# Performance work log

Measured on AMD Instinct MI355X. Metric: run time of the kernel, lower is better.

The kernel has to match this reference:

```python
import jax, jax.numpy as jnp
import numpy as np

N = 50000
E = 800000
IN = 128
HID = 128
OUT = 128
HEADS = 8
EPS = 1e-5
NEG_SLOPE = 0.2


def _gat_conv(x, src, dst, W, a_src, a_dst, b, concat):
    """PyG-style GATConv (eval mode, self-loops already appended to src/dst).
    W: [Fin, H*C], a_src/a_dst: [H, C], b: [H*C] or [C]."""
    n = x.shape[0]
    H, C = a_src.shape
    h = (x @ W).reshape(n, H, C)                      # [N,H,C]
    al_s = jnp.einsum('nhc,hc->nh', h, a_src)         # [N,H]
    al_d = jnp.einsum('nhc,hc->nh', h, a_dst)         # [N,H]
    e = jax.nn.leaky_relu(al_s[src] + al_d[dst], NEG_SLOPE)  # [E',H]
    m = jax.ops.segment_max(e, dst, num_segments=n)   # per-dst softmax (stable)
    ex = jnp.exp(e - m[dst])
    s = jax.ops.segment_sum(ex, dst, num_segments=n)
    alpha = ex / s[dst]                               # [E',H]
    out = jax.ops.segment_sum(h[src] * alpha[..., None], dst, num_segments=n)
    out = out.reshape(n, H * C) if concat else out[:, 0, :]
    return out + b


def _layernorm(x, g, b):
    mu = x.mean(-1, keepdims=True)
    var = ((x - mu) ** 2).mean(-1, keepdims=True)
    return (x - mu) * jax.lax.rsqrt(var + EPS) * g + b


def setup_inputs() -> dict:
    key = jax.random.key(0)
    ks = jax.random.split(key, 24)
    d = {}
    d['x'] = jax.random.normal(ks[0], (N, IN), jnp.float32)
    d['edge_index'] = jax.random.randint(ks[1], (2, E), 0, N)
    C = HID // HEADS
    # layer 0: in -> hidden, 8 heads, concat
    d['W0'] = jax.random.normal(ks[2], (IN, HID)) * 0.05
    d['a_src0'] = jax.random.normal(ks[3], (HEADS, C)) * 0.05
    d['a_dst0'] = jax.random.normal(ks[4], (HEADS, C)) * 0.05
    d['b0'] = jnp.zeros((HID,), jnp.float32)
    d['g0'] = jnp.ones((HID,), jnp.float32)
    d['be0'] = jnp.zeros((HID,), jnp.float32)
    # layer 1: hidden -> hidden, 8 heads, concat
    d['W1'] = jax.random.normal(ks[5], (HID, HID)) * 0.05
    d['a_src1'] = jax.random.normal(ks[6], (HEADS, C)) * 0.05
    d['a_dst1'] = jax.random.normal(ks[7], (HEADS, C)) * 0.05
    d['b1'] = jnp.zeros((HID,), jnp.float32)
    d['g1'] = jnp.ones((HID,), jnp.float32)
    d['be1'] = jnp.zeros((HID,), jnp.float32)
    # layer 2: hidden -> out, 1 head, no concat
    d['W2'] = jax.random.normal(ks[8], (HID, OUT)) * 0.05
    d['a_src2'] = jax.random.normal(ks[9], (1, OUT)) * 0.05
    d['a_dst2'] = jax.random.normal(ks[10], (1, OUT)) * 0.05
    d['b2'] = jnp.zeros((OUT,), jnp.float32)
    d['g2'] = jnp.ones((OUT,), jnp.float32)
    d['be2'] = jnp.zeros((OUT,), jnp.float32)
    return d


def reference(x, edge_index, W0, a_src0, a_dst0, b0, g0, be0,
              W1, a_src1, a_dst1, b1, g1, be1,
              W2, a_src2, a_dst2, b2, g2, be2):
    n = x.shape[0]
    loops = jnp.arange(n)
    src = jnp.concatenate([edge_index[0], loops])  # add self-loops (PyG default)
    dst = jnp.concatenate([edge_index[1], loops])

    h = _gat_conv(x, src, dst, W0, a_src0, a_dst0, b0, concat=True)
    h = jax.nn.elu(_layernorm(h, g0, be0))          # dropout: eval mode -> identity
    h = _gat_conv(h, src, dst, W1, a_src1, a_dst1, b1, concat=True)
    h = jax.nn.elu(_layernorm(h, g1, be1))
    h = _gat_conv(h, src, dst, W2, a_src2, a_dst2, b2, concat=False)
    h = _layernorm(h, g2, be2)
    return h
```

## Files before the change

kernel.cpp:

```cpp
#include <hip/hip_runtime.h>
#include <hip/hip_bf16.h>

#define NN 50000
#define EE 800000
#define EP 850000
#define DD 128
#define NB 196

#define NBUCK 196
#define BCAP 8192
#define E_PER_BLK 4096

typedef __attribute__((ext_vector_type(8))) short short8;
typedef __attribute__((ext_vector_type(4))) float f32x4;

__device__ __forceinline__ float bfu(unsigned short u){ return __uint_as_float(((unsigned)u)<<16); }
__device__ __forceinline__ unsigned short f2bs(float x){
  __hip_bfloat16 h = __float2bfloat16(x);
  union { __hip_bfloat16 h; unsigned short u; } cv; cv.h = h; return cv.u;
}

__global__ void __launch_bounds__(256) prep_kernel(
    const float* __restrict__ W0, const float* __restrict__ as0, const float* __restrict__ ad0,
    const float* __restrict__ W1, const float* __restrict__ as1, const float* __restrict__ ad1,
    const float* __restrict__ W2, const float* __restrict__ as2, const float* __restrict__ ad2,
    unsigned short* __restrict__ Wmf, int* __restrict__ bcur)
{
  const int tid = threadIdx.x;
  if (blockIdx.x == 0 && tid < NBUCK) bcur[tid] = 0;
  if (blockIdx.x < 24){
    const int L = blockIdx.x >> 3, seg = blockIdx.x & 7;
    const float* W = (L == 0) ? W0 : (L == 1) ? W1 : W2;
    int idx = seg*256 + tid;
    int t = idx >> 6, lane = idx & 63;
    int c = t >> 2, kb = t & 3;
    int m = lane & 15, quad = lane >> 4;
    unsigned short out[8];
    #pragma unroll
    for (int j = 0; j < 8; j++){
      int k = kb*32 + quad*8 + j;
      out[j] = f2bs(W[(size_t)k*DD + c*16 + m]);
    }
    *(uint4*)&Wmf[(((size_t)L*36 + t)*64 + lane)*8] = *(const uint4*)out;
  } else if (blockIdx.x < 120){
    const int q = blockIdx.x - 24;
    const int wIdx = q*4 + (tid >> 6);
    const int L = wIdx >> 7, k = wIdx & 127;
    const float *W, *as, *ad; int H;
    if (L == 0){ W = W0; as = as0; ad = ad0; H = 8; }
    else if (L == 1){ W = W1; as = as1; ad = ad1; H = 8; }
    else { W = W2; as = as2; ad = ad2; H = 1; }
    const int lane = tid & 63;
    const int c0 = lane*2;
    float w0 = W[(size_t)k*DD + c0];
    float w1 = W[(size_t)k*DD + c0 + 1];
    float ps = w0*as[c0] + w1*as[c0+1];
    float pd = w0*ad[c0] + w1*ad[c0+1];
    if (H == 8){
      #pragma unroll
      for (int off = 1; off <= 4; off <<= 1){
        ps += __shfl_xor(ps, off, 64);
        pd += __shfl_xor(pd, off, 64);
      }
    } else {
      #pragma unroll
      for (int off = 1; off <= 32; off <<= 1){
        ps += __shfl_xor(ps, off, 64);
        pd += __shfl_xor(pd, off, 64);
      }
    }
    int srcLane = (lane < 8) ? lane*8 : (lane < 16 ? (lane-8)*8 : 0);
    float vs = __shfl(ps, srcLane, 64);
    float vd = __shfl(pd, srcLane, 64);
    float myv;
    if (H == 8) myv = (lane < 8) ? vs : (lane < 16 ? vd : 0.f);
    else        myv = (lane == 0) ? ps : (lane == 1 ? pd : 0.f);
    const int kb = k >> 5, quad = (k >> 3) & 3, j = k & 7;
    if (lane < 16)
      Wmf[(((size_t)L*36 + 32 + kb)*64 + quad*16 + lane)*8 + j] = f2bs(myv);
  }
}

__global__ void __launch_bounds__(256) binpass1_kernel(const int* __restrict__ ei,
    unsigned int* __restrict__ bins, int* __restrict__ bcur)
{
  __shared__ int h[NBUCK];
  __shared__ int lofs[NBUCK];
  __shared__ int gbase[NBUCK];
  __shared__ unsigned int st[E_PER_BLK];
  __shared__ int buf[256];
  const int tid = threadIdx.x;
  for (int i = tid; i < NBUCK; i += 256) h[i] = 0;
  __syncthreads();

  const int e0 = blockIdx.x * E_PER_BLK;
  unsigned int pk[16];
  #pragma unroll
  for (int k = 0; k < 16; k++){
    int e = e0 + k*256 + tid;
    if (e < EP){
      int s, d;
      if (e < EE){ s = ei[e]; d = ei[EE + e]; } else { s = d = e - EE; }
      int b = d >> 8;
      pk[k] = ((unsigned)s << 16) | ((unsigned)b << 8) | (unsigned)(d & 255);
      atomicAdd(&h[b], 1);
    } else pk[k] = 0xFFFFFFFFu;
  }
  __syncthreads();

  int v = (tid < NBUCK) ? h[tid] : 0;
  buf[tid] = v;
  __syncthreads();
  for (int off = 1; off < 256; off <<= 1){
    int t = (tid >= off) ? buf[tid - off] : 0;
    __syncthreads();
    buf[tid] += t;
    __syncthreads();
  }
  if (tid < NBUCK){
    lofs[tid]  = buf[tid] - v;
    gbase[tid] = (v > 0) ? atomicAdd(&bcur[tid], v) : 0;
    h[tid] = lofs[tid];
  }
  __syncthreads();

  #pragma unroll
  for (int k = 0; k < 16; k++){
    if (pk[k] != 0xFFFFFFFFu){
      int b = (pk[k] >> 8) & 255;
      int p = atomicAdd(&h[b], 1);
      st[p] = pk[k];
    }
  }
  __syncthreads();

  const int total = buf[255];
  for (int i = tid; i < total; i += 256){
    unsigned int p = st[i];
    int b = (p >> 8) & 255;
    int idx = gbase[b] + (i - lofs[b]);
    if (idx < BCAP) bins[(size_t)b * BCAP + idx] = p;
  }
}

__global__ void __launch_bounds__(256) binpass2_kernel(const unsigned int* __restrict__ bins,
    const int* __restrict__ bcur, int* __restrict__ rowStart, unsigned short* __restrict__ srcL)
{
  __shared__ int buf[256];
  __shared__ int lcnt[256];
  __shared__ int lcur[256];
  __shared__ int ebase_s, cnt_s;
  const int b = blockIdx.x;
  const int tid = threadIdx.x;

  int v = (tid < NBUCK) ? bcur[tid] : 0;
  buf[tid] = v;
  lcnt[tid] = 0;
  __syncthreads();
  for (int off = 1; off < 256; off <<= 1){
    int t = (tid >= off) ? buf[tid - off] : 0;
    __syncthreads();
    buf[tid] += t;
    __syncthreads();
  }
  if (tid == b){ ebase_s = buf[tid] - v; cnt_s = v; }
  __syncthreads();
  const int ebase = ebase_s, cnt = cnt_s;
  const unsigned int* mybins = bins + (size_t)b * BCAP;

  for (int i = tid; i < cnt; i += 256)
    atomicAdd(&lcnt[mybins[i] & 255], 1);
  __syncthreads();

  int c = lcnt[tid];
  buf[tid] = c;
  __syncthreads();
  for (int off = 1; off < 256; off <<= 1){
    int t = (tid >= off) ? buf[tid - off] : 0;
    __syncthreads();
    buf[tid] += t;
    __syncthreads();
  }
  int excl = buf[tid] - c;
  int d = (b << 8) + tid;
  if (d <= NN) rowStart[d] = ebase + excl;
  lcur[tid] = ebase + excl;
  __syncthreads();

  for (int i = tid; i < cnt; i += 256){
    unsigned int p = mybins[i];
    int pos = atomicAdd(&lcur[p & 255], 1);
    srcL[pos] = (unsigned short)(p >> 16);
  }
}

template<bool XBF16, int H>
__global__ void __launch_bounds__(256) gemm_mfma_kernel(const void* __restrict__ Xv,
    const unsigned short* __restrict__ Wmf,
    unsigned short* __restrict__ Hout,
    float* __restrict__ alS, float* __restrict__ alD)
{
  __shared__ unsigned short wl[36*64*8];
  const int tid = threadIdx.x;
  {
    const uint4* src = (const uint4*)Wmf;
    uint4* dst = (uint4*)wl;
    #pragma unroll
    for (int i = 0; i < 9; i++)
      dst[tid + i*256] = src[tid + i*256];
  }
  const int lane = tid & 63, wv = tid >> 6;
  const int r0 = blockIdx.x*64 + wv*16;
  const int m = lane & 15, quad = lane >> 4;
  const int row = r0 + m;
  const bool rowOK = row < NN;

  short8 a[4];
  if (XBF16){
    const short* Xb = (const short*)Xv;
    #pragma unroll
    for (int kb = 0; kb < 4; kb++){
      if (rowOK) a[kb] = *(const short8*)&Xb[(size_t)row*DD + kb*32 + quad*8];
      else       a[kb] = (short8){0,0,0,0,0,0,0,0};
    }
  } else {
    const float* Xf = (const float*)Xv;
    #pragma unroll
    for (int kb = 0; kb < 4; kb++){
      if (rowOK){
        float4 f0 = *(const float4*)&Xf[(size_t)row*DD + kb*32 + quad*8];
        float4 f1 = *(const float4*)&Xf[(size_t)row*DD + kb*32 + quad*8 + 4];
        union { short8 v; unsigned short u[8]; } cv;
        cv.u[0]=f2bs(f0.x); cv.u[1]=f2bs(f0.y); cv.u[2]=f2bs(f0.z); cv.u[3]=f2bs(f0.w);
        cv.u[4]=f2bs(f1.x); cv.u[5]=f2bs(f1.y); cv.u[6]=f2bs(f1.z); cv.u[7]=f2bs(f1.w);
        a[kb] = cv.v;
      } else a[kb] = (short8){0,0,0,0,0,0,0,0};
    }
  }
  __syncthreads();

  f32x4 acc[9];
  #pragma unroll
  for (int c = 0; c < 9; c++) acc[c] = (f32x4){0.f,0.f,0.f,0.f};
  #pragma unroll
  for (int c = 0; c < 9; c++){
    #pragma unroll
    for (int kb = 0; kb < 4; kb++){
      short8 b = *(const short8*)&wl[((c*4 + kb)*64 + lane)*8];
      acc[c] = __builtin_amdgcn_mfma_f32_16x16x32_bf16(a[kb], b, acc[c], 0, 0, 0);
    }
  }

  #pragma unroll
  for (int c = 0; c < 8; c++){
    #pragma unroll
    for (int r = 0; r < 4; r++){
      int rw = r0 + quad*4 + r;
      if (rw < NN) Hout[(size_t)rw*DD + c*16 + m] = f2bs(acc[c][r]);
    }
  }
  #pragma unroll
  for (int r = 0; r < 4; r++){
    int rw = r0 + quad*4 + r;
    if (rw < NN){
      float v = acc[8][r];
      if (H == 8){
        if (m < 8) alS[rw*8 + m]       = v;
        else       alD[rw*8 + (m - 8)] = v;
      } else {
        if (m == 0)      alS[rw] = v;
        else if (m == 1) alD[rw] = v;
      }
    }
  }
}

template<int H, bool FINAL>
__global__ void __launch_bounds__(256) aggln_kernel(
    const int* __restrict__ rowStart, const unsigned short* __restrict__ srcL,
    const float* __restrict__ alS, const float* __restrict__ alD,
    const unsigned short* __restrict__ hB,
    const float* __restrict__ b, const float* __restrict__ g, const float* __restrict__ be,
    void* __restrict__ outv)
{
  const int lane = threadIdx.x & 63;
  const int d    = blockIdx.x*4 + (threadIdx.x >> 6);
  const int C    = DD / H;
  const int c0   = lane*2;
  const int hd   = c0 / C;
  const int start = __builtin_amdgcn_readfirstlane(rowStart[d]);
  const int end   = __builtin_amdgcn_readfirstlane(rowStart[d+1]);
  const float aldv = alD[d*H + hd];

  float ssum = 0.f, a0 = 0.f, a1 = 0.f;
  const unsigned int* __restrict__ sw = (const unsigned int*)srcL;

  #define PROC(sv) { \
    int s_ = (sv); \
    const unsigned short* hr_ = hB + (size_t)s_*DD; \
    const float* ar_ = alS + s_*H; \
    unsigned int hw_ = *(const unsigned int*)&hr_[c0]; \
    float e_ = ar_[hd] + aldv; \
    e_ = fmaxf(e_, 0.2f*e_); \
    float w_ = __expf(e_); \
    ssum += w_; \
    a0 = fmaf(__uint_as_float(hw_ << 16),          w_, a0); \
    a1 = fmaf(__uint_as_float(hw_ & 0xFFFF0000u),  w_, a1); \
  }

  int jw = start >> 1;
  if (start & 1){
    unsigned int w = sw[jw]; PROC((int)(w >> 16)); jw++;
  }
  const int jwF = end >> 1;
  for (; jw + 2 <= jwF; jw += 2){
    unsigned int w0 = sw[jw], w1 = sw[jw+1];
    PROC((int)(w0 & 0xFFFFu)); PROC((int)(w0 >> 16));
    PROC((int)(w1 & 0xFFFFu)); PROC((int)(w1 >> 16));
  }
  for (; jw < jwF; ++jw){
    unsigned int w = sw[jw];
    PROC((int)(w & 0xFFFFu)); PROC((int)(w >> 16));
  }
  if (end & 1){
    unsigned int w = sw[jwF]; PROC((int)(w & 0xFFFFu));
  }
  #undef PROC

  const float sinv = 1.f / ssum;

  float v0 = a0*sinv + b[c0], v1 = a1*sinv + b[c0+1];
  float s2 = v0 + v1;
  #pragma unroll
  for (int off = 32; off >= 1; off >>= 1) s2 += __shfl_xor(s2, off, 64);
  float mu = s2 * (1.0f/128.0f);
  float d0 = v0 - mu, d1 = v1 - mu;
  float q = d0*d0 + d1*d1;
  #pragma unroll
  for (int off = 32; off >= 1; off >>= 1) q += __shfl_xor(q, off, 64);
  float r = rsqrtf(q*(1.0f/128.0f) + 1e-5f);
  float y0 = d0*r*g[c0]   + be[c0];
  float y1 = d1*r*g[c0+1] + be[c0+1];
  if (FINAL){
    *(float2*)&((float*)outv)[(size_t)d*DD + c0] = make_float2(y0, y1);
  } else {
    y0 = y0 > 0.f ? y0 : __expf(y0) - 1.f;
    y1 = y1 > 0.f ? y1 : __expf(y1) - 1.f;
    ushort2 o; o.x = f2bs(y0); o.y = f2bs(y1);
    *(ushort2*)&((unsigned short*)outv)[(size_t)d*DD + c0] = o;
  }
}

template<bool XBF16, int H, bool FINAL>
static void run_layer(const void* x, const unsigned short* WmfL,
                      const float* b, const float* g, const float* be,
                      const int* rowStart, const unsigned short* srcL,
                      unsigned short* hB, float* alS, float* alD,
                      void* outv, hipStream_t stream)
{
  gemm_mfma_kernel<XBF16, H><<<782, 256, 0, stream>>>(x, WmfL, hB, alS, alD);
  aggln_kernel<H, FINAL><<<12500, 256, 0, stream>>>(rowStart, srcL, alS, alD, hB,
                                                    b, g, be, outv);
}

extern "C" void kernel_launch(void* const* d_in, const int* in_sizes, int n_in,
                              void* d_out, int out_size, void* d_ws, size_t ws_size,
                              hipStream_t stream)
{
  char* w = (char*)d_ws;
  unsigned short* accB = (unsigned short*)w;     w += (size_t)NN*DD*2;
  unsigned short* hB   = (unsigned short*)w;     w += (size_t)NN*DD*2;
  float* alS      = (float*)w;                   w += (size_t)NN*8*4;
  float* alD      = (float*)w;                   w += (size_t)NN*8*4;
  unsigned short* Wmf = (unsigned short*)w;      w += (size_t)3*36*64*8*2;
  int*   rowStart = (int*)w;                     w += (size_t)(NN+1)*4;
  int*   bcur     = (int*)w;                     w += 1024;
  unsigned short* srcL = (unsigned short*)w;     w += (size_t)EP*2;
  if (ws_size < (size_t)(w - (char*)d_ws)) return;

  unsigned int* bins = (unsigned int*)accB;

  const float* x  = (const float*)d_in[0];
  const int*   ei = (const int*)d_in[1];
  const float *W0=(const float*)d_in[2], *as0=(const float*)d_in[3], *ad0=(const float*)d_in[4];
  const float *b0=(const float*)d_in[5], *g0=(const float*)d_in[6], *be0=(const float*)d_in[7];
  const float *W1=(const float*)d_in[8], *as1=(const float*)d_in[9], *ad1=(const float*)d_in[10];
  const float *b1=(const float*)d_in[11],*g1=(const float*)d_in[12],*be1=(const float*)d_in[13];
  const float *W2=(const float*)d_in[14],*as2=(const float*)d_in[15],*ad2=(const float*)d_in[16];
  const float *b2=(const float*)d_in[17],*g2=(const float*)d_in[18],*be2=(const float*)d_in[19];

  prep_kernel<<<NB, 256, 0, stream>>>(W0, as0, ad0, W1, as1, ad1, W2, as2, ad2, Wmf, bcur);
  binpass1_kernel<<<(EP + E_PER_BLK - 1)/E_PER_BLK, 256, 0, stream>>>(ei, bins, bcur);
  binpass2_kernel<<<NBUCK, 256, 0, stream>>>(bins, bcur, rowStart, srcL);

  run_layer<false, 8, false>(x,    Wmf,            b0, g0, be0,
                             rowStart, srcL, hB, alS, alD, accB, stream);
  run_layer<true, 8, false>(accB, Wmf + (size_t)36*64*8,   b1, g1, be1,
                             rowStart, srcL, hB, alS, alD, accB, stream);
  run_layer<true, 1, true>(accB, Wmf + (size_t)2*36*64*8,  b2, g2, be2,
                             rowStart, srcL, hB, alS, alD, d_out, stream);
}
```

Baseline: 284.0 us.

## Fuse layer-0 GEMM with edge binning pass and batch gather loads in aggregation

The first layer's MFMA GEMM and the first edge-binning pass now run as one launch, with blocks split by index and a shared LDS buffer, so the two independent stages overlap and one launch is saved. The aggregation kernel now loads up to 127 source indices per wave with one coalesced read and broadcasts them with readlane. It then issues eight independent gathers of features and attention scores before doing the math, to raise memory-level parallelism. This costs more registers and relies on the hand-computed LDS offsets and the 127-edge chunk bound being correct.

```diff
diff --git a/kernel.cpp b/kernel.cpp
--- a/kernel.cpp
+++ b/kernel.cpp
@@ -10,6 +10,8 @@
 #define NBUCK 196
 #define BCAP 8192
 #define E_PER_BLK 4096
+#define GEMM_BLKS 782
+#define BP1_BLKS ((EP + E_PER_BLK - 1)/E_PER_BLK)
 
 typedef __attribute__((ext_vector_type(8))) short short8;
 typedef __attribute__((ext_vector_type(4))) float f32x4;
@@ -81,19 +83,19 @@
   }
 }
 
-__global__ void __launch_bounds__(256) binpass1_kernel(const int* __restrict__ ei,
-    unsigned int* __restrict__ bins, int* __restrict__ bcur)
-{
-  __shared__ int h[NBUCK];
-  __shared__ int lofs[NBUCK];
-  __shared__ int gbase[NBUCK];
-  __shared__ unsigned int st[E_PER_BLK];
-  __shared__ int buf[256];
+__device__ __forceinline__ void bp1_body(int bid, const int* __restrict__ ei,
+    unsigned int* __restrict__ bins, int* __restrict__ bcur, char* smem)
+{
+  unsigned int* st = (unsigned int*)smem;
+  int* h     = (int*)(smem + 16384);
+  int* lofs  = (int*)(smem + 17168);
+  int* gbase = (int*)(smem + 17952);
+  int* buf   = (int*)(smem + 18736);
   const int tid = threadIdx.x;
   for (int i = tid; i < NBUCK; i += 256) h[i] = 0;
   __syncthreads();
 
-  const int e0 = blockIdx.x * E_PER_BLK;
+  const int e0 = bid * E_PER_BLK;
   unsigned int pk[16];
   #pragma unroll
   for (int k = 0; k < 16; k++){
@@ -195,12 +197,12 @@
 }
 
 template<bool XBF16, int H>
-__global__ void __launch_bounds__(256) gemm_mfma_kernel(const void* __restrict__ Xv,
+__device__ __forceinline__ void gemm_body(int bid, const void* __restrict__ Xv,
     const unsigned short* __restrict__ Wmf,
     unsigned short* __restrict__ Hout,
-    float* __restrict__ alS, float* __restrict__ alD)
-{
-  __shared__ unsigned short wl[36*64*8];
+    float* __restrict__ alS, float* __restrict__ alD,
+    unsigned short* wl)
+{
   const int tid = threadIdx.x;
   {
     const uint4* src = (const uint4*)Wmf;
@@ -210,7 +212,7 @@
       dst[tid + i*256] = src[tid + i*256];
   }
   const int lane = tid & 63, wv = tid >> 6;
-  const int r0 = blockIdx.x*64 + wv*16;
+  const int r0 = bid*64 + wv*16;
   const int m = lane & 15, quad = lane >> 4;
   const int row = r0 + m;
   const bool rowOK = row < NN;
@@ -275,6 +277,30 @@
   }
 }
 
+template<bool XBF16, int H>
+__global__ void __launch_bounds__(256) gemm_mfma_kernel(const void* __restrict__ Xv,
+    const unsigned short* __restrict__ Wmf,
+    unsigned short* __restrict__ Hout,
+    float* __restrict__ alS, float* __restrict__ alD)
+{
+  __shared__ unsigned short wl[36*64*8];
+  gemm_body<XBF16, H>(blockIdx.x, Xv, Wmf, Hout, alS, alD, wl);
+}
+
+template<bool XBF16, int H>
+__global__ void __launch_bounds__(256) gemm_bp1_kernel(const void* __restrict__ Xv,
+    const unsigned short* __restrict__ Wmf,
+    unsigned short* __restrict__ Hout,
+    float* __restrict__ alS, float* __restrict__ alD,
+    const int* __restrict__ ei, unsigned int* __restrict__ bins, int* __restrict__ bcur)
+{
+  __shared__ __align__(16) char smem[36*64*8*2];
+  if (blockIdx.x < GEMM_BLKS)
+    gemm_body<XBF16, H>(blockIdx.x, Xv, Wmf, Hout, alS, alD, (unsigned short*)smem);
+  else
+    bp1_body(blockIdx.x - GEMM_BLKS, ei, bins, bcur, smem);
+}
+
 template<int H, bool FINAL>
 __global__ void __launch_bounds__(256) aggln_kernel(
     const int* __restrict__ rowStart, const unsigned short* __restrict__ srcL,
@@ -295,37 +321,51 @@
   float ssum = 0.f, a0 = 0.f, a1 = 0.f;
   const unsigned int* __restrict__ sw = (const unsigned int*)srcL;
 
-  #define PROC(sv) { \
-    int s_ = (sv); \
-    const unsigned short* hr_ = hB + (size_t)s_*DD; \
-    const float* ar_ = alS + s_*H; \
-    unsigned int hw_ = *(const unsigned int*)&hr_[c0]; \
-    float e_ = ar_[hd] + aldv; \
-    e_ = fmaxf(e_, 0.2f*e_); \
-    float w_ = __expf(e_); \
-    ssum += w_; \
-    a0 = fmaf(__uint_as_float(hw_ << 16),          w_, a0); \
-    a1 = fmaf(__uint_as_float(hw_ & 0xFFFF0000u),  w_, a1); \
-  }
-
-  int jw = start >> 1;
-  if (start & 1){
-    unsigned int w = sw[jw]; PROC((int)(w >> 16)); jw++;
-  }
-  const int jwF = end >> 1;
-  for (; jw + 2 <= jwF; jw += 2){
-    unsigned int w0 = sw[jw], w1 = sw[jw+1];
-    PROC((int)(w0 & 0xFFFFu)); PROC((int)(w0 >> 16));
-    PROC((int)(w1 & 0xFFFFu)); PROC((int)(w1 >> 16));
-  }
-  for (; jw < jwF; ++jw){
-    unsigned int w = sw[jw];
-    PROC((int)(w & 0xFFFFu)); PROC((int)(w >> 16));
-  }
-  if (end & 1){
-    unsigned int w = sw[jwF]; PROC((int)(w & 0xFFFFu));
-  }
-  #undef PROC
+  int base = start;
+  while (base < end){
+    const int cnt = min(127, end - base);
+    const int jw0 = base >> 1;
+    unsigned int myW = (jw0 + lane < (EP >> 1)) ? sw[jw0 + lane] : 0u;
+
+    int k = 0;
+    for (; k + 8 <= cnt; k += 8){
+      int ss[8];
+      #pragma unroll
+      for (int i = 0; i < 8; i++){
+        int eidx = base + k + i;
+        unsigned int wv = (unsigned int)__builtin_amdgcn_readlane((int)myW, (eidx >> 1) - jw0);
+        ss[i] = (eidx & 1) ? (int)(wv >> 16) : (int)(wv & 0xFFFFu);
+      }
+      unsigned int hw[8]; float av[8];
+      #pragma unroll
+      for (int i = 0; i < 8; i++) hw[i] = *(const unsigned int*)&hB[(size_t)ss[i]*DD + c0];
+      #pragma unroll
+      for (int i = 0; i < 8; i++) av[i] = alS[ss[i]*H + hd];
+      #pragma unroll
+      for (int i = 0; i < 8; i++){
+        float e_ = av[i] + aldv;
+        e_ = fmaxf(e_, 0.2f*e_);
+        float w_ = __expf(e_);
+        ssum += w_;
+        a0 = fmaf(__uint_as_float(hw[i] << 16),         w_, a0);
+        a1 = fmaf(__uint_as_float(hw[i] & 0xFFFF0000u), w_, a1);
+      }
+    }
+    for (; k < cnt; k++){
+      int eidx = base + k;
+      unsigned int wv = (unsigned int)__builtin_amdgcn_readlane((int)myW, (eidx >> 1) - jw0);
+      int s_ = (eidx & 1) ? (int)(wv >> 16) : (int)(wv & 0xFFFFu);
+      unsigned int hw_ = *(const unsigned int*)&hB[(size_t)s_*DD + c0];
+      float av_ = alS[s_*H + hd];
+      float e_ = av_ + aldv;
+      e_ = fmaxf(e_, 0.2f*e_);
+      float w_ = __expf(e_);
+      ssum += w_;
+      a0 = fmaf(__uint_as_float(hw_ << 16),         w_, a0);
+      a1 = fmaf(__uint_as_float(hw_ & 0xFFFF0000u), w_, a1);
+    }
+    base += cnt;
+  }
 
   const float sinv = 1.f / ssum;
 
@@ -351,18 +391,6 @@
   }
 }
 
-template<bool XBF16, int H, bool FINAL>
-static void run_layer(const void* x, const unsigned short* WmfL,
-                      const float* b, const float* g, const float* be,
-                      const int* rowStart, const unsigned short* srcL,
-                      unsigned short* hB, float* alS, float* alD,
-                      void* outv, hipStream_t stream)
-{
-  gemm_mfma_kernel<XBF16, H><<<782, 256, 0, stream>>>(x, WmfL, hB, alS, alD);
-  aggln_kernel<H, FINAL><<<12500, 256, 0, stream>>>(rowStart, srcL, alS, alD, hB,
-                                                    b, g, be, outv);
-}
-
 extern "C" void kernel_launch(void* const* d_in, const int* in_sizes, int n_in,
                               void* d_out, int out_size, void* d_ws, size_t ws_size,
                               hipStream_t stream)
@@ -390,13 +418,19 @@
   const float *b2=(const float*)d_in[17],*g2=(const float*)d_in[18],*be2=(const float*)d_in[19];
 
   prep_kernel<<<NB, 256, 0, stream>>>(W0, as0, ad0, W1, as1, ad1, W2, as2, ad2, Wmf, bcur);
-  binpass1_kernel<<<(EP + E_PER_BLK - 1)/E_PER_BLK, 256, 0, stream>>>(ei, bins, bcur);
+
+  gemm_bp1_kernel<false, 8><<<GEMM_BLKS + BP1_BLKS, 256, 0, stream>>>(
+      x, Wmf, hB, alS, alD, ei, bins, bcur);
   binpass2_kernel<<<NBUCK, 256, 0, stream>>>(bins, bcur, rowStart, srcL);
 
-  run_layer<false, 8, false>(x,    Wmf,            b0, g0, be0,
-                             rowStart, srcL, hB, alS, alD, accB, stream);
-  run_layer<true, 8, false>(accB, Wmf + (size_t)36*64*8,   b1, g1, be1,
-                             rowStart, srcL, hB, alS, alD, accB, stream);
-  run_layer<true, 1, true>(accB, Wmf + (size_t)2*36*64*8,  b2, g2, be2,
-                             rowStart, srcL, hB, alS, alD, d_out, stream);
-}
+  aggln_kernel<8, false><<<12500, 256, 0, stream>>>(rowStart, srcL, alS, alD, hB,
+                                                    b0, g0, be0, accB);
+  gemm_mfma_kernel<true, 8><<<GEMM_BLKS, 256, 0, stream>>>(accB, Wmf + (size_t)36*64*8,
+                                                           hB, alS, alD);
+  aggln_kernel<8, false><<<12500, 256, 0, stream>>>(rowStart, srcL, alS, alD, hB,
+                                                    b1, g1, be1, accB);
+  gemm_mfma_kernel<true, 1><<<GEMM_BLKS, 256, 0, stream>>>(accB, Wmf + (size_t)2*36*64*8,
+                                                           hB, alS, alD);
+  aggln_kernel<1, true><<<12500, 256, 0, stream>>>(rowStart, srcL, alS, alD, hB,
+                                                   b2, g2, be2, d_out);
+}
```

Result: no change. 284.7 us (+0.2%).
